# Kernel optimization log

Hardware: AMD Instinct MI355X
Metric: run time of the kernel (lower is better)

## Reference

```python
import jax, jax.numpy as jnp
import numpy as np

HEADS = 8
DIM_HEAD = 64
SCALE = DIM_HEAD ** (-0.5)


def setup_inputs() -> dict:
    key = jax.random.key(0)
    k1, k2, k3 = jax.random.split(key, 3)
    b, l, c = 8, 4096, 512
    x = jax.random.normal(k1, (b, l, c), dtype=jnp.float32)
    w_qkv = jax.random.normal(k2, (3 * c, c), dtype=jnp.float32) * (c ** -0.5)
    w_out = jax.random.normal(k3, (c, c), dtype=jnp.float32) * (c ** -0.5)
    b_out = jnp.zeros((c,), dtype=jnp.float32)
    return {"x": x, "w_qkv": w_qkv, "w_out": w_out, "b_out": b_out}


def reference(x, w_qkv, w_out, b_out):
    b, l, c = x.shape
    h = HEADS
    lh = l // h
    # to_qkv: Linear(dim, 3*dim, bias=False)
    qkv = x @ w_qkv.T                                   # (b, l, 3c)
    qkv = qkv.reshape(b, lh, h, 3, c).transpose(3, 0, 2, 1, 4)  # (3, b, h, l/h, c)
    q, k, v = qkv[0], qkv[1], qkv[2]                    # each (b, h, l/h, c)
    # transpose(-2,-1): attention is over the CHANNEL axis
    q = jnp.swapaxes(q, -2, -1)                         # (b, h, c, l/h)
    k = jnp.swapaxes(k, -2, -1)                         # (b, h, c, l/h)
    v = jnp.swapaxes(v, -2, -1)                         # (b, h, c, l/h)
    attn = jnp.einsum('bhcl,bhdl->bhcd', q, k) * SCALE  # (b, h, c, c)
    attn = jax.nn.softmax(attn, axis=-1)
    y = jnp.einsum('bhcd,bhdl->bhcl', attn, v)          # (b, h, c, l/h)
    y = y.transpose(0, 3, 1, 2).reshape(b, l, c)        # (b, l/h, h, c) -> (b, l, c)
    # to_out: Linear(dim, dim) + Dropout (identity at eval)
    out = y @ w_out.T + b_out
    return out
```

## Files before the change

### kernel.cpp

```cpp
#include <hip/hip_runtime.h>
#include <stdint.h>
#include <stddef.h>

typedef _Float16 f16;
typedef _Float16 f16x8 __attribute__((ext_vector_type(8)));
typedef _Float16 f16x4 __attribute__((ext_vector_type(4)));
typedef float f32x4 __attribute__((ext_vector_type(4)));

__device__ __forceinline__ void gload16(const void* g, void* l) {
    auto gp = (const __attribute__((address_space(1))) uint32_t*)(uintptr_t)g;
    auto lp = (__attribute__((address_space(3))) uint32_t*)(uintptr_t)l;
    __builtin_amdgcn_global_load_lds(gp, lp, 16, 0, 0);
}

__device__ __forceinline__ f16x4 cvt4(f32x4 v) {
    return f16x4{ (f16)v[0], (f16)v[1], (f16)v[2], (f16)v[3] };
}

__global__ __launch_bounds__(256) void prep_k(const float* __restrict__ x,
                                              const float* __restrict__ wqkv,
                                              const float* __restrict__ wout,
                                              f16* __restrict__ xb,
                                              f16* __restrict__ wqb,
                                              f16* __restrict__ wob) {
    int tid = blockIdx.x * blockDim.x + threadIdx.x;
    int stride = gridDim.x * blockDim.x;
    for (int i = tid; i < 4194304; i += stride) {
        float4 v = ((const float4*)x)[i];
        *(f16x4*)(xb + (size_t)i * 4) = f16x4{ (f16)v.x, (f16)v.y, (f16)v.z, (f16)v.w };
    }
    for (int i = tid; i < 196608; i += stride) {
        float4 v = ((const float4*)wqkv)[i];
        *(f16x4*)(wqb + (size_t)i * 4) = f16x4{ (f16)v.x, (f16)v.y, (f16)v.z, (f16)v.w };
    }
    for (int i = tid; i < 65536; i += stride) {
        float4 v = ((const float4*)wout)[i];
        *(f16x4*)(wob + (size_t)i * 4) = f16x4{ (f16)v.x, (f16)v.y, (f16)v.z, (f16)v.w };
    }
}


#define STAGE(NB) do {                                                          \
    gload16(At + soff,          &ldsA[NB][(  0 + wid*8)*64]);                   \
    gload16(At + soff + 65536,  &ldsA[NB][( 64 + wid*8)*64]);                   \
    gload16(At + soff + 131072, &ldsA[NB][(128 + wid*8)*64]);                   \
    gload16(At + soff + 196608, &ldsA[NB][(192 + wid*8)*64]);                   \
    gload16(Bt + soff,          &ldsB[NB][(  0 + wid*8)*64]);                   \
    gload16(Bt + soff + 65536,  &ldsB[NB][( 64 + wid*8)*64]);                   \
    gload16(Bt + soff + 131072, &ldsB[NB][(128 + wid*8)*64]);                   \
    gload16(Bt + soff + 196608, &ldsB[NB][(192 + wid*8)*64]);                   \
    At += 128; Bt += 128;                                                       \
} while (0)

#define RD(BUF) do {                                                            \
    _Pragma("unroll") for (int ni = 0; ni < 4; ++ni)                            \
    _Pragma("unroll") for (int kk = 0; kk < 2; ++kk)                            \
        bF[ni][kk] = *(const f16x8*)(&ldsB[BUF][0] + boff[ni] + kk * 32);       \
    _Pragma("unroll") for (int mi = 0; mi < 8; ++mi)                            \
    _Pragma("unroll") for (int kk = 0; kk < 2; ++kk)                            \
        aF[mi][kk] = *(const f16x8*)(&ldsA[BUF][0] + aoff[mi] + kk * 32);       \
} while (0)

#define MM do {                                                                 \
    __builtin_amdgcn_s_setprio(1);                                              \
    _Pragma("unroll") for (int mi = 0; mi < 8; ++mi)                            \
    _Pragma("unroll") for (int ni = 0; ni < 4; ++ni)                            \
    _Pragma("unroll") for (int kk = 0; kk < 2; ++kk) {                          \
        if constexpr (SWP)                                                      \
            acc[mi][ni] = __builtin_amdgcn_mfma_f32_16x16x32_f16(               \
                bF[ni][kk], aF[mi][kk], acc[mi][ni], 0, 0, 0);                  \
        else                                                                    \
            acc[mi][ni] = __builtin_amdgcn_mfma_f32_16x16x32_f16(               \
                aF[mi][kk], bF[ni][kk], acc[mi][ni], 0, 0, 0);                  \
    }                                                                           \
    __builtin_amdgcn_s_setprio(0);                                              \
} while (0)

#define W0  asm volatile("s_waitcnt vmcnt(0)" ::: "memory")
#define BAR __builtin_amdgcn_s_barrier()

#define TILE(CB, NB, STG, FINAL) do {                                           \
    if (STG) STAGE(NB);                                                         \
    RD(CB);                                                                     \
    MM;                                                                         \
    if (!FINAL) { W0; BAR; }                                                    \
} while (0)

template <int MODE, bool SWP, bool QK>
__global__ __launch_bounds__(512, 2) void g11_k(const f16* __restrict__ A0,
                                                const f16* __restrict__ B0,
                                                void* __restrict__ C0,
                                                void* __restrict__ C1,
                                                const float* __restrict__ bias) {
    __shared__ f16 ldsA[2][16384];
    __shared__ f16 ldsB[2][16384];

    const int tid = threadIdx.x;
    const int lane = tid & 63;
    const int wid = tid >> 6;
    const int wr = wid >> 2;
    const int wc = wid & 3;

    const int bid = blockIdx.x;
    int tm, tn, bh = 0;
    if constexpr (MODE == 0 && QK) {
        int swz = (bid & 7) * 64 + (bid >> 3);
        tm = (swz >> 2) * 256; tn = (swz & 3) * 256;
    } else if constexpr (MODE == 0) {
        int swz = (bid & 7) * 32 + (bid >> 3);
        tm = (swz >> 1) * 256; tn = (swz & 1) * 256;
    } else if constexpr (MODE == 1 || MODE == 2) {
        int swz = (bid & 7) * 32 + (bid >> 3);
        bh = swz >> 2; tm = ((swz >> 1) & 1) * 256; tn = (swz & 1) * 256;
    } else {
        int swz = (bid & 7) * 32 + (bid >> 3);
        tm = (swz >> 1) * 256; tn = (swz & 1) * 256;
    }

    const size_t bhoff = (MODE == 1 || MODE == 2) ? (size_t)bh * 262144 : 0;
    const char* At = (const char*)(A0 + bhoff + (size_t)tm * 512);
    const char* Bt = (const char*)(B0 + bhoff + (size_t)tn * 512);

    const int soff = wid * 8192 + (lane >> 3) * 1024 +
                     (((lane & 7) ^ ((lane >> 3) & 3) ^ (wid & 3)) * 16);

    int aoff[8], boff[4];
#pragma unroll
    for (int mi = 0; mi < 8; ++mi) {
        int r;
        if constexpr (QK) {
            r = wr * 128 + (lane & 15) * 8 + mi;
        } else {
            r = wr * 128 + mi * 16 + (lane & 15);
        }
        int s2 = (r & 3) ^ ((r >> 3) & 3);
        aoff[mi] = r * 64 + (((lane >> 4) ^ s2)) * 8;
    }
#pragma unroll
    for (int ni = 0; ni < 4; ++ni) {
        int r = wc * 64 + ni * 16 + (lane & 15);
        int s2 = (r & 3) ^ ((r >> 3) & 3);
        boff[ni] = r * 64 + (((lane >> 4) ^ s2)) * 8;
    }

    f32x4 acc[8][4] = {};
    f16x8 aF[8][2], bF[4][2];

    STAGE(0);
    W0; BAR;

#pragma unroll 1
    for (int i = 0; i < 3; ++i) {
        TILE(0, 1, true, false);
        TILE(1, 0, true, false);
    }
    TILE(0, 1, true, false);
    TILE(1, 1, false, true);

    if constexpr (MODE == 0 && QK) {
        const int b = tm >> 12;
        const int lt = (tm & 4095) >> 3;
        f16* dst = (f16*)(tn < 512 ? C0 : C1);
        const int cb = (tn & 511) + wc * 64;
        const int lh0 = lt + wr * 16 + (lane >> 4) * 4;
#pragma unroll
        for (int mi = 0; mi < 8; ++mi) {
            int h = mi;
#pragma unroll
            for (int ni = 0; ni < 4; ++ni) {
                int c = cb + ni * 16 + (lane & 15);
                *(f16x4*)(dst + ((size_t)((b * 8 + h) * 512 + c)) * 512 + lh0) =
                    cvt4(acc[mi][ni]);
            }
        }
    } else if constexpr (MODE == 0) {
        f16* dst = (f16*)C0;
#pragma unroll
        for (int mi = 0; mi < 8; ++mi) {
            int t = tm + wr * 128 + mi * 16 + (lane & 15);
            int b = t >> 12, l = t & 4095;
            int h = l & 7, lh = l >> 3;
#pragma unroll
            for (int ni = 0; ni < 4; ++ni) {
                int d0 = tn + wc * 64 + ni * 16 + (lane >> 4) * 4;
                *(f16x4*)(dst + ((size_t)((b * 8 + h) * 512 + lh)) * 512 + d0) =
                    cvt4(acc[mi][ni]);
            }
        }
    } else if constexpr (MODE == 1) {
        f16* S = (f16*)C0 + (size_t)bh * 262144;
#pragma unroll
        for (int mi = 0; mi < 8; ++mi) {
            int cm = tm + wr * 128 + mi * 16 + (lane & 15);
#pragma unroll
            for (int ni = 0; ni < 4; ++ni) {
                int d0 = tn + wc * 64 + ni * 16 + (lane >> 4) * 4;
                *(f16x4*)(S + (size_t)cm * 512 + d0) = cvt4(acc[mi][ni] * 0.125f);
            }
        }
    } else if constexpr (MODE == 2) {
        f16* yb = (f16*)C0;
        const int b = bh >> 3, h = bh & 7;
#pragma unroll
        for (int mi = 0; mi < 8; ++mi) {
            int c0 = tm + wr * 128 + mi * 16 + (lane >> 4) * 4;
#pragma unroll
            for (int ni = 0; ni < 4; ++ni) {
                int l = tn + wc * 64 + ni * 16 + (lane & 15);
                size_t tok = (size_t)b * 4096 + (size_t)l * 8 + h;
                *(f16x4*)(yb + tok * 512 + c0) = cvt4(acc[mi][ni]);
            }
        }
    } else {
        float* O = (float*)C0;
#pragma unroll
        for (int mi = 0; mi < 8; ++mi) {
            int m = tm + wr * 128 + mi * 16 + (lane & 15);
#pragma unroll
            for (int ni = 0; ni < 4; ++ni) {
                int n0 = tn + wc * 64 + ni * 16 + (lane >> 4) * 4;
                float4 bv = *(const float4*)(bias + n0);
                f32x4 v = acc[mi][ni];
                v[0] += bv.x; v[1] += bv.y; v[2] += bv.z; v[3] += bv.w;
                *(f32x4*)(O + (size_t)m * 512 + n0) = v;
            }
        }
    }
}

__global__ __launch_bounds__(256) void softmax_k(const f16* __restrict__ S,
                                                 f16* __restrict__ P) {
    int row = blockIdx.x * 4 + (threadIdx.x >> 6);
    int lane = threadIdx.x & 63;
    f16x8 v = *(const f16x8*)(S + (size_t)row * 512 + lane * 8);
    float f[8];
#pragma unroll
    for (int i = 0; i < 8; ++i) f[i] = (float)v[i];
    float m = f[0];
#pragma unroll
    for (int i = 1; i < 8; ++i) m = fmaxf(m, f[i]);
#pragma unroll
    for (int off = 1; off < 64; off <<= 1) m = fmaxf(m, __shfl_xor(m, off, 64));
    float s = 0.f, e[8];
#pragma unroll
    for (int i = 0; i < 8; ++i) { e[i] = __expf(f[i] - m); s += e[i]; }
#pragma unroll
    for (int off = 1; off < 64; off <<= 1) s += __shfl_xor(s, off, 64);
    float inv = 1.0f / s;
    f16x8 pk;
#pragma unroll
    for (int i = 0; i < 8; ++i) pk[i] = (f16)(e[i] * inv);
    *(f16x8*)(P + (size_t)row * 512 + lane * 8) = pk;
}

extern "C" void kernel_launch(void* const* d_in, const int* in_sizes, int n_in,
                              void* d_out, int out_size, void* d_ws, size_t ws_size,
                              hipStream_t stream) {
    const float* x = (const float*)d_in[0];
    const float* wqkv = (const float*)d_in[1];
    const float* wout = (const float*)d_in[2];
    const float* bout = (const float*)d_in[3];
    float* out = (float*)d_out;
    char* ws = (char*)d_ws;
    const size_t MBs = 1u << 20;

    f16* xb  = (f16*)(ws + 0);
    f16* wqb = (f16*)(ws + 32 * MBs);
    f16* wob = (f16*)(ws + 34 * MBs);
    f16* Qb  = (f16*)(ws + 35 * MBs);
    f16* Kb  = (f16*)(ws + 67 * MBs);
    f16* Vb  = (f16*)(ws + 99 * MBs);
    f16* Sb  = (f16*)(ws + 131 * MBs);
    f16* Pb  = xb;
    f16* yb  = Qb;

    prep_k<<<1024, 256, 0, stream>>>(x, wqkv, wout, xb, wqb, wob);
    g11_k<0, false, true><<<512, 512, 0, stream>>>(xb, wqb, Qb, Kb, nullptr);
    g11_k<0, true, false><<<256, 512, 0, stream>>>(xb, wqb + (size_t)1024 * 512, Vb, nullptr, nullptr);
    g11_k<1, true, false><<<256, 512, 0, stream>>>(Qb, Kb, Sb, nullptr, nullptr);
    softmax_k<<<8192, 256, 0, stream>>>(Sb, Pb);
    g11_k<2, false, false><<<256, 512, 0, stream>>>(Pb, Vb, yb, nullptr, nullptr);
    g11_k<3, true, false><<<256, 512, 0, stream>>>(yb, wob, out, nullptr, bout);
}
```

Before: 201.6 us.

## Split LDS fragment reads into k-halves, widen swizzle, drop occupancy hint

Each 64-wide K tile is now read from LDS in two 32-wide halves, and MFMAs on the first half overlap the issue of the next stage's global loads and the reads of the second half. Fragment registers are halved, which relieves register pressure. The LDS XOR swizzle goes from 2 bits to 3 bits to cut bank conflicts. The launch_bounds minimum of 2 blocks per CU is removed, which may change how many waves the compiler allows per CU.

```diff
diff --git a/kernel.cpp b/kernel.cpp
--- a/kernel.cpp
+++ b/kernel.cpp
@@ -52,26 +52,23 @@
     At += 128; Bt += 128;                                                       \
 } while (0)
 
-#define RD(BUF) do {                                                            \
+#define RD12(KK, BUF) do {                                                      \
     _Pragma("unroll") for (int ni = 0; ni < 4; ++ni)                            \
-    _Pragma("unroll") for (int kk = 0; kk < 2; ++kk)                            \
-        bF[ni][kk] = *(const f16x8*)(&ldsB[BUF][0] + boff[ni] + kk * 32);       \
+        bF[ni] = *(const f16x8*)(&ldsB[BUF][0] + boff[ni][KK]);                 \
     _Pragma("unroll") for (int mi = 0; mi < 8; ++mi)                            \
-    _Pragma("unroll") for (int kk = 0; kk < 2; ++kk)                            \
-        aF[mi][kk] = *(const f16x8*)(&ldsA[BUF][0] + aoff[mi] + kk * 32);       \
-} while (0)
-
-#define MM do {                                                                 \
+        aF[mi] = *(const f16x8*)(&ldsA[BUF][0] + aoff[mi][KK]);                 \
+} while (0)
+
+#define MM32 do {                                                               \
     __builtin_amdgcn_s_setprio(1);                                              \
     _Pragma("unroll") for (int mi = 0; mi < 8; ++mi)                            \
-    _Pragma("unroll") for (int ni = 0; ni < 4; ++ni)                            \
-    _Pragma("unroll") for (int kk = 0; kk < 2; ++kk) {                          \
+    _Pragma("unroll") for (int ni = 0; ni < 4; ++ni) {                          \
         if constexpr (SWP)                                                      \
             acc[mi][ni] = __builtin_amdgcn_mfma_f32_16x16x32_f16(               \
-                bF[ni][kk], aF[mi][kk], acc[mi][ni], 0, 0, 0);                  \
+                bF[ni], aF[mi], acc[mi][ni], 0, 0, 0);                          \
         else                                                                    \
             acc[mi][ni] = __builtin_amdgcn_mfma_f32_16x16x32_f16(               \
-                aF[mi][kk], bF[ni][kk], acc[mi][ni], 0, 0, 0);                  \
+                aF[mi], bF[ni], acc[mi][ni], 0, 0, 0);                          \
     }                                                                           \
     __builtin_amdgcn_s_setprio(0);                                              \
 } while (0)
@@ -80,18 +77,20 @@
 #define BAR __builtin_amdgcn_s_barrier()
 
 #define TILE(CB, NB, STG, FINAL) do {                                           \
+    RD12(0, CB);                                                                \
     if (STG) STAGE(NB);                                                         \
-    RD(CB);                                                                     \
-    MM;                                                                         \
+    MM32;                                                                       \
+    RD12(1, CB);                                                                \
+    MM32;                                                                       \
     if (!FINAL) { W0; BAR; }                                                    \
 } while (0)
 
 template <int MODE, bool SWP, bool QK>
-__global__ __launch_bounds__(512, 2) void g11_k(const f16* __restrict__ A0,
-                                                const f16* __restrict__ B0,
-                                                void* __restrict__ C0,
-                                                void* __restrict__ C1,
-                                                const float* __restrict__ bias) {
+__global__ __launch_bounds__(512) void g12_k(const f16* __restrict__ A0,
+                                             const f16* __restrict__ B0,
+                                             void* __restrict__ C0,
+                                             void* __restrict__ C1,
+                                             const float* __restrict__ bias) {
     __shared__ f16 ldsA[2][16384];
     __shared__ f16 ldsB[2][16384];
 
@@ -122,9 +121,9 @@
     const char* Bt = (const char*)(B0 + bhoff + (size_t)tn * 512);
 
     const int soff = wid * 8192 + (lane >> 3) * 1024 +
-                     (((lane & 7) ^ ((lane >> 3) & 3) ^ (wid & 3)) * 16);
-
-    int aoff[8], boff[4];
+                     ((((lane & 7) ^ (lane >> 3) ^ wid) & 7) * 16);
+
+    int aoff[8][2], boff[4][2];
 #pragma unroll
     for (int mi = 0; mi < 8; ++mi) {
         int r;
@@ -133,18 +132,22 @@
         } else {
             r = wr * 128 + mi * 16 + (lane & 15);
         }
-        int s2 = (r & 3) ^ ((r >> 3) & 3);
-        aoff[mi] = r * 64 + (((lane >> 4) ^ s2)) * 8;
+        int s3 = (r & 7) ^ ((r >> 3) & 7);
+#pragma unroll
+        for (int kk = 0; kk < 2; ++kk)
+            aoff[mi][kk] = r * 64 + ((((lane >> 4) + kk * 4) ^ s3)) * 8;
     }
 #pragma unroll
     for (int ni = 0; ni < 4; ++ni) {
         int r = wc * 64 + ni * 16 + (lane & 15);
-        int s2 = (r & 3) ^ ((r >> 3) & 3);
-        boff[ni] = r * 64 + (((lane >> 4) ^ s2)) * 8;
+        int s3 = (r & 7) ^ ((r >> 3) & 7);
+#pragma unroll
+        for (int kk = 0; kk < 2; ++kk)
+            boff[ni][kk] = r * 64 + ((((lane >> 4) + kk * 4) ^ s3)) * 8;
     }
 
     f32x4 acc[8][4] = {};
-    f16x8 aF[8][2], bF[4][2];
+    f16x8 aF[8], bF[4];
 
     STAGE(0);
     W0; BAR;
@@ -275,10 +278,10 @@
     f16* yb  = Qb;
 
     prep_k<<<1024, 256, 0, stream>>>(x, wqkv, wout, xb, wqb, wob);
-    g11_k<0, false, true><<<512, 512, 0, stream>>>(xb, wqb, Qb, Kb, nullptr);
-    g11_k<0, true, false><<<256, 512, 0, stream>>>(xb, wqb + (size_t)1024 * 512, Vb, nullptr, nullptr);
-    g11_k<1, true, false><<<256, 512, 0, stream>>>(Qb, Kb, Sb, nullptr, nullptr);
+    g12_k<0, false, true><<<512, 512, 0, stream>>>(xb, wqb, Qb, Kb, nullptr);
+    g12_k<0, true, false><<<256, 512, 0, stream>>>(xb, wqb + (size_t)1024 * 512, Vb, nullptr, nullptr);
+    g12_k<1, true, false><<<256, 512, 0, stream>>>(Qb, Kb, Sb, nullptr, nullptr);
     softmax_k<<<8192, 256, 0, stream>>>(Sb, Pb);
-    g11_k<2, false, false><<<256, 512, 0, stream>>>(Pb, Vb, yb, nullptr, nullptr);
-    g11_k<3, true, false><<<256, 512, 0, stream>>>(yb, wob, out, nullptr, bout);
-}
+    g12_k<2, false, false><<<256, 512, 0, stream>>>(Pb, Vb, yb, nullptr, nullptr);
+    g12_k<3, true, false><<<256, 512, 0, stream>>>(yb, wob, out, nullptr, bout);
+}
```

Measured after the change: 190.4 us. -5.6%, faster.
